# Performance work log

Hardware: AMD Instinct MI355X
Metric: run time of the kernel (lower is better)

Reference implementation:

```python
import jax, jax.numpy as jnp
import numpy as np

PRED_LEN = 256
K = 32
LOW_FREQ = 1


def setup_inputs() -> dict:
    key = jax.random.key(0)
    x = jax.random.normal(key, (8, 1024, 512), dtype=jnp.float32)
    return {"x": x}


def _fourier_layer(x):
    b, t, d = x.shape
    # per-channel standardization over time (torch .std is unbiased -> ddof=1)
    x_mean = jnp.mean(x, axis=1, keepdims=True)                      # (b,1,d)
    x_std = jnp.std(x, axis=1, keepdims=True, ddof=1) + 1e-8         # (b,1,d)
    xs = jnp.clip((x - x_mean) / x_std, -2.0, 2.0) + 1e-9

    # rfft over time; t is even and LOW_FREQ < t//2 -> drop DC..low_freq-1 and Nyquist
    x_freq = jnp.fft.rfft(xs, axis=1)[:, LOW_FREQ:-1]                # (b,N,d) complex64
    n_freq = x_freq.shape[1]
    f = jnp.fft.rfftfreq(t).astype(jnp.float32)[LOW_FREQ:n_freq + LOW_FREQ]  # (N,)

    # top-k frequencies by amplitude, independently per (batch, channel)
    amp_all = jnp.abs(x_freq).astype(jnp.float32)                    # (b,N,d)
    _, idx = jax.lax.top_k(jnp.transpose(amp_all, (0, 2, 1)), K)     # (b,d,k)
    idx = jnp.transpose(idx, (0, 2, 1))                              # (b,k,d)
    xf = jnp.take_along_axis(x_freq, idx, axis=1)                    # (b,k,d)
    f_sel = f[idx]                                                   # (b,k,d)

    # extrapolate: conjugate pair -> real signal, sum of k cosines
    xf2 = jnp.concatenate([xf, jnp.conj(xf)], axis=1)                # (b,2k,d)
    f2 = jnp.concatenate([f_sel, -f_sel], axis=1)[:, :, None, :]     # (b,2k,1,d)
    T = t + PRED_LEN
    t_val = jnp.arange(T, dtype=jnp.float32)[None, None, :, None]    # (1,1,T,1)
    amp = (jnp.abs(xf2) / (t + 1e-8))[:, :, None, :]                 # (b,2k,1,d)
    phase = jnp.clip(jnp.angle(xf2), -np.pi, np.pi)[:, :, None, :]   # (b,2k,1,d)
    angle = 2.0 * np.pi * f2 * t_val + phase                         # (b,2k,T,d)
    angle = angle - 2.0 * np.pi * jnp.floor(angle / (2.0 * np.pi))
    x_time = jnp.sum(amp * jnp.cos(angle), axis=1)                   # (b,T,d)

    return x_time * x_std + x_mean


def reference(x):
    return _fourier_layer(x)
```

## Files before the change

kernel.cpp:

```cpp
#include <hip/hip_runtime.h>

#define T_IN 1024
#define D_DIM 512
#define T_OUT 1280
#define NPAIR 4096

__global__ __launch_bounds__(256) void transpose_kernel(const float* __restrict__ x,
                                                        float* __restrict__ xt,
                                                        double2* __restrict__ tw) {
    __shared__ float tile[64][65];
    const int b  = blockIdx.z;
    const int t0 = blockIdx.y * 64;
    const int d0 = blockIdx.x * 64;
    const int dl = threadIdx.x & 63;
    const int r0 = threadIdx.x >> 6;

    if (blockIdx.x < 4 && blockIdx.y == 0 && blockIdx.z == 0) {
        int m = blockIdx.x * 256 + threadIdx.x;
        double th = (6.283185307179586476925286766559 / 1024.0) * (double)m;
        tw[m] = make_double2(cos(th), -sin(th));
    }

#pragma unroll
    for (int i = 0; i < 16; ++i) {
        int tl = r0 * 16 + i;
        tile[tl][dl] = x[((size_t)b * T_IN + (t0 + tl)) * D_DIM + d0 + dl];
    }
    __syncthreads();
#pragma unroll
    for (int i = 0; i < 16; ++i) {
        int dl2 = r0 * 16 + i;
        xt[((size_t)b * D_DIM + (d0 + dl2)) * T_IN + t0 + dl] = tile[dl][dl2];
    }
}

__device__ __forceinline__ double2 TW16(const double2* __restrict__ E, int m) {
    const double RS2 = 0.70710678118654752440084436210485;
    int r = m & 255;
    int q = (m >> 8) & 3;
    int r2 = (r <= 128) ? r : 256 - r;
    double cc, ss;
    if (r2 <= 64) {
        double2 t = E[r2];
        cc = t.x; ss = t.y;
    } else {
        double2 t = E[128 - r2];
        cc = (t.x + t.y) * RS2;
        ss = (t.x - t.y) * RS2;
    }
    double c, s;
    if (r > 128) { c = ss; s = cc; } else { c = cc; s = ss; }
    double C, S;
    switch (q) {
        case 0:  C = c;  S = s;  break;
        case 1:  C = -s; S = c;  break;
        case 2:  C = -c; S = -s; break;
        default: C = s;  S = -c; break;
    }
    return make_double2(C, -S);
}

__global__ __launch_bounds__(256) void dft_kernel(const float* __restrict__ xt,
                                                  const double2* __restrict__ twg,
                                                  float2* __restrict__ stats,
                                                  float4* __restrict__ sel) {
    __shared__ double2 uni[1024];
    __shared__ double2 tw_s[65];
    __shared__ double2 w32_s[32];
    __shared__ double  red_s[16];
    double* xs_s = (double*)uni;

    const int tid  = threadIdx.x;
    const int pair = blockIdx.x;

    const float4 v = reinterpret_cast<const float4*>(xt + (size_t)pair * T_IN)[tid];

    if (tid < 65) {
        double2 t = twg[tid];
        tw_s[tid] = make_double2(t.x, -t.y);
    }
    if (tid >= 128 && tid < 160) {
        w32_s[tid - 128] = twg[(tid - 128) * 32];
    }

    double sum = (double)v.x + (double)v.y + (double)v.z + (double)v.w;
    double sq  = (double)v.x * v.x + (double)v.y * v.y +
                 (double)v.z * v.z + (double)v.w * v.w;
#pragma unroll
    for (int off = 32; off; off >>= 1) {
        sum += __shfl_down(sum, off);
        sq  += __shfl_down(sq, off);
    }
    const int wv   = tid >> 6;
    const int lane = tid & 63;
    if (lane == 0) { red_s[wv] = sum; red_s[8 + wv] = sq; }
    __syncthreads();
    double mean, stdp;
    {
        double s = red_s[0] + red_s[1] + red_s[2] + red_s[3];
        double q = red_s[8] + red_s[9] + red_s[10] + red_s[11];
        mean = s * (1.0 / 1024.0);
        double var = (q - 1024.0 * mean * mean) * (1.0 / 1023.0);
        var = var > 0.0 ? var : 0.0;
        stdp = sqrt(var) + 1e-8;
        if (tid == 0) stats[pair] = make_float2((float)mean, (float)stdp);
    }
    const double inv = 1.0 / stdp;
    {
        double z0 = ((double)v.x - mean) * inv;
        double z1 = ((double)v.y - mean) * inv;
        double z2 = ((double)v.z - mean) * inv;
        double z3 = ((double)v.w - mean) * inv;
        z0 = fmin(2.0, fmax(-2.0, z0)) + 1e-9;
        z1 = fmin(2.0, fmax(-2.0, z1)) + 1e-9;
        z2 = fmin(2.0, fmax(-2.0, z2)) + 1e-9;
        z3 = fmin(2.0, fmax(-2.0, z3)) + 1e-9;
        xs_s[tid * 4 + 0] = z0;
        xs_s[tid * 4 + 1] = z1;
        xs_s[tid * 4 + 2] = z2;
        xs_s[tid * 4 + 3] = z3;
    }
    __syncthreads();

    {
        int idx = tid;
#pragma unroll
        for (int rr = 0; rr < 2; ++rr) {
            if (idx < 480) {
                int t1p = 1 + (idx >> 5);
                int t2c = idx & 31;
                int ia = t1p * 32 + t2c;
                int ib = (32 - t1p) * 32 + t2c;
                double a = xs_s[ia], b = xs_s[ib];
                xs_s[ia] = a + b;
                xs_s[ib] = a - b;
            }
            idx += 256;
        }
    }
    __syncthreads();

    const int k1 = tid & 31;
    const int g  = tid >> 5;

    double2 R0, R1, R2, R3;
    {
        const double sgn16 = (k1 & 1) ? -1.0 : 1.0;

        double ar0 = xs_s[g]      + sgn16 * xs_s[512 + g];
        double ar1 = xs_s[g + 8]  + sgn16 * xs_s[512 + g + 8];
        double ar2 = xs_s[g + 16] + sgn16 * xs_s[512 + g + 16];
        double ar3 = xs_s[g + 24] + sgn16 * xs_s[512 + g + 24];
        double ai0 = 0, ai1 = 0, ai2 = 0, ai3 = 0;

        int jw = 0;
#pragma unroll 5
        for (int t1 = 1; t1 <= 15; ++t1) {
            jw = (jw + k1) & 31;
            double2 w = w32_s[jw];
            const double* eb = &xs_s[t1 * 32];
            const double* ob = &xs_s[(32 - t1) * 32];
            ar0 = fma(eb[g], w.x, ar0);      ai0 = fma(ob[g], w.y, ai0);
            ar1 = fma(eb[g + 8], w.x, ar1);  ai1 = fma(ob[g + 8], w.y, ai1);
            ar2 = fma(eb[g + 16], w.x, ar2); ai2 = fma(ob[g + 16], w.y, ai2);
            ar3 = fma(eb[g + 24], w.x, ar3); ai3 = fma(ob[g + 24], w.y, ai3);
        }
        {
            double2 tm = TW16(tw_s, g * k1);
            R0 = make_double2(ar0 * tm.x - ai0 * tm.y, ar0 * tm.y + ai0 * tm.x);
        }
        {
            double2 tm = TW16(tw_s, (g + 8) * k1);
            R1 = make_double2(ar1 * tm.x - ai1 * tm.y, ar1 * tm.y + ai1 * tm.x);
        }
        {
            double2 tm = TW16(tw_s, (g + 16) * k1);
            R2 = make_double2(ar2 * tm.x - ai2 * tm.y, ar2 * tm.y + ai2 * tm.x);
        }
        {
            double2 tm = TW16(tw_s, (g + 24) * k1);
            R3 = make_double2(ar3 * tm.x - ai3 * tm.y, ar3 * tm.y + ai3 * tm.x);
        }
    }
    __syncthreads();

    uni[g * 32 + k1]        = make_double2(R0.x + R2.x, R0.y + R2.y);
    uni[(g + 16) * 32 + k1] = make_double2(R0.x - R2.x, R0.y - R2.y);
    uni[(g + 8) * 32 + k1]  = make_double2(R1.x + R3.x, R1.y + R3.y);
    uni[(g + 24) * 32 + k1] = make_double2(R1.x - R3.x, R1.y - R3.y);
    __syncthreads();

    double Ar = 0, Ai = 0, Br = 0, Bi = 0;
    {
        const int ebase = (g & 1) ? 16 * 32 : 0;
        int ja = 0;
#pragma unroll
        for (int u = 0; u < 4; ++u) {
            {
                double2 w = w32_s[ja]; ja = (ja + g) & 31;
                double2 E = uni[ebase + (4 * u + 0) * 32 + k1];
                double P = fma(E.x, w.x, -(E.y * w.y));
                double Q = fma(E.x, w.y,  (E.y * w.x));
                Ar += P; Ai += Q; Br += P; Bi += Q;
            }
            {
                double2 w = w32_s[ja]; ja = (ja + g) & 31;
                double2 E = uni[ebase + (4 * u + 1) * 32 + k1];
                double P = fma(E.x, w.x, -(E.y * w.y));
                double Q = fma(E.x, w.y,  (E.y * w.x));
                Ar += P; Ai += Q; Br += Q; Bi -= P;
            }
            {
                double2 w = w32_s[ja]; ja = (ja + g) & 31;
                double2 E = uni[ebase + (4 * u + 2) * 32 + k1];
                double P = fma(E.x, w.x, -(E.y * w.y));
                double Q = fma(E.x, w.y,  (E.y * w.x));
                Ar += P; Ai += Q; Br -= P; Bi -= Q;
            }
            {
                double2 w = w32_s[ja]; ja = (ja + g) & 31;
                double2 E = uni[ebase + (4 * u + 3) * 32 + k1];
                double P = fma(E.x, w.x, -(E.y * w.y));
                double Q = fma(E.x, w.y,  (E.y * w.x));
                Ar += P; Ai += Q; Br -= Q; Bi += P;
            }
        }
    }
    const int ka = k1 + 32 * g;
    const int kb = ka + 256;

    unsigned long long uA, uB;
    {
        double a2a = Ar * Ar + Ai * Ai;
        double a2b = Br * Br + Bi * Bi;
        unsigned long long bba = __double_as_longlong(a2a);
        unsigned long long bbb = __double_as_longlong(a2b);
        double keya = __longlong_as_double((bba & ~1023ULL) |
                                           (unsigned long long)(1023 - ka));
        double keyb = __longlong_as_double((bbb & ~1023ULL) |
                                           (unsigned long long)(1023 - kb));
        if (ka == 0) keya = -1.0;
        unsigned long long a = (unsigned long long)__double_as_longlong(keya);
        unsigned long long b = (unsigned long long)__double_as_longlong(keyb);
        uA = a ^ ((a >> 63) ? 0xFFFFFFFFFFFFFFFFULL : 0x8000000000000000ULL);
        uB = b ^ ((b >> 63) ? 0xFFFFFFFFFFFFFFFFULL : 0x8000000000000000ULL);
    }

    __syncthreads();
    float2* spec_f = (float2*)uni;
    double* cand   = (double*)(uni + 512);
    spec_f[ka] = make_float2((float)Ar, (float)Ai);
    spec_f[kb] = make_float2((float)Br, (float)Bi);

    const unsigned long long lt = lane ? (0xFFFFFFFFFFFFFFFFULL >> (64 - lane))
                                       : 0ULL;

    {
        const unsigned int aHi = (unsigned int)(uA >> 32);
        const unsigned int bHi = (unsigned int)(uB >> 32);
        unsigned int pref = 0x80000000u;
#pragma unroll
        for (int bit = 30; bit >= 0; --bit) {
            unsigned int trial = pref | (1u << bit);
            int cnt = __popcll(__ballot(aHi >= trial)) +
                      __popcll(__ballot(bHi >= trial));
            if (cnt >= 32) pref = trial;
        }
        unsigned long long gA = __ballot(aHi > pref);
        unsigned long long gB = __ballot(bHi > pref);
        unsigned long long eA = __ballot(aHi == pref);
        unsigned long long eB = __ballot(bHi == pref);
        int nH = __popcll(gA) + __popcll(gB);
        int nE = __popcll(eA) + __popcll(eB);
        bool winA, winB;
        if (nH + nE == 32) {
            winA = (aHi >= pref);
            winB = (bHi >= pref);
        } else {
            const unsigned int aLo = (unsigned int)uA;
            const unsigned int bLo = (unsigned int)uB;
            int need = 32 - nH;
            unsigned int lp = 0;
            for (int bit = 31; bit >= 0; --bit) {
                unsigned int t = lp | (1u << bit);
                int c = __popcll(__ballot((aHi == pref) && (aLo >= t))) +
                        __popcll(__ballot((bHi == pref) && (bLo >= t)));
                if (c >= need) lp = t;
            }
            winA = (aHi > pref) || ((aHi == pref) && (aLo >= lp));
            winB = (bHi > pref) || ((bHi == pref) && (bLo >= lp));
        }
        unsigned long long mA = __ballot(winA);
        unsigned long long mB = __ballot(winB);
        const int bs = wv * 32;
        if (winA)
            cand[bs + __popcll(mA & lt)] = __longlong_as_double((long long)uA);
        if (winB)
            cand[bs + __popcll(mA) + __popcll(mB & lt)] =
                __longlong_as_double((long long)uB);
    }
    __syncthreads();

    if (tid < 64) {
        unsigned long long c0 =
            (unsigned long long)__double_as_longlong(cand[tid]);
        unsigned long long c1 =
            (unsigned long long)__double_as_longlong(cand[tid + 64]);
        const unsigned int h0 = (unsigned int)(c0 >> 32);
        const unsigned int h1 = (unsigned int)(c1 >> 32);
        unsigned int pref = 0x80000000u;
#pragma unroll
        for (int bit = 30; bit >= 0; --bit) {
            unsigned int trial = pref | (1u << bit);
            int cnt = __popcll(__ballot(h0 >= trial)) +
                      __popcll(__ballot(h1 >= trial));
            if (cnt >= 32) pref = trial;
        }
        unsigned long long g0 = __ballot(h0 > pref);
        unsigned long long g1 = __ballot(h1 > pref);
        unsigned long long e0 = __ballot(h0 == pref);
        unsigned long long e1 = __ballot(h1 == pref);
        int nH = __popcll(g0) + __popcll(g1);
        int nE = __popcll(e0) + __popcll(e1);
        bool win0, win1;
        if (nH + nE == 32) {
            win0 = (h0 >= pref);
            win1 = (h1 >= pref);
        } else {
            const unsigned int l0 = (unsigned int)c0;
            const unsigned int l1 = (unsigned int)c1;
            int need = 32 - nH;
            unsigned int lp = 0;
            for (int bit = 31; bit >= 0; --bit) {
                unsigned int t = lp | (1u << bit);
                int c = __popcll(__ballot((h0 == pref) && (l0 >= t))) +
                        __popcll(__ballot((h1 == pref) && (l1 >= t)));
                if (c >= need) lp = t;
            }
            win0 = (h0 > pref) || ((h0 == pref) && (l0 >= lp));
            win1 = (h1 > pref) || ((h1 == pref) && (l1 >= lp));
        }
        unsigned long long m0 = __ballot(win0);
        unsigned long long m1 = __ballot(win1);
        const float C = 6.28318530717958647692f / 1024.0f;
        const size_t sb = (size_t)pair * 32;
        if (win0) {
            int slot = __popcll(m0 & lt);
            int k = 1023 - (int)(c0 & 1023ULL);
            float2 sp = spec_f[k];
            float ph = atan2f(sp.y, sp.x);
            double key = __longlong_as_double(
                (long long)(c0 ^ 0x8000000000000000ULL));
            double amp = sqrt(key);
            float aout = (float)(2.0 * amp / (1024.0 + 1e-8));
            float tkc = __cosf((float)k * C);
            sel[sb + slot] = make_float4(aout, ph, (float)k, tkc);
        }
        if (win1) {
            int slot = __popcll(m0) + __popcll(m1 & lt);
            int k = 1023 - (int)(c1 & 1023ULL);
            float2 sp = spec_f[k];
            float ph = atan2f(sp.y, sp.x);
            double key = __longlong_as_double(
                (long long)(c1 ^ 0x8000000000000000ULL));
            double amp = sqrt(key);
            float aout = (float)(2.0 * amp / (1024.0 + 1e-8));
            float tkc = __cosf((float)k * C);
            sel[sb + slot] = make_float4(aout, ph, (float)k, tkc);
        }
    }
}

__global__ __launch_bounds__(256) void recon_kernel(const float4* __restrict__ sel,
                                                    const float2* __restrict__ stats,
                                                    float* __restrict__ out) {
    __shared__ float4 sel_s[32][65];
    __shared__ float2 st_s[64];
    const int bid   = blockIdx.x;
    const int chunk = bid & 15;
    const int dt    = (bid >> 4) & 7;
    const int b     = bid >> 7;
    const int d0    = dt * 64;
    const int tid   = threadIdx.x;
#pragma unroll
    for (int it = 0; it < 8; ++it) {
        int i   = tid + it * 256;
        int j   = i & 31;
        int dls = i >> 5;
        sel_s[j][dls] = sel[((size_t)(b * D_DIM + d0 + dls)) * 32 + j];
    }
    if (tid < 64) st_s[tid] = stats[b * D_DIM + d0 + tid];
    __syncthreads();

    const int dl    = tid & 63;
    const int wvv   = tid >> 6;
    const int tbase = chunk * 64 + wvv * 16;

    float acc[16];
#pragma unroll
    for (int j = 0; j < 16; ++j) acc[j] = 0.0f;

    const float C = 6.28318530717958647692f / 1024.0f;
#pragma unroll 2
    for (int js = 0; js < 32; ++js) {
        float4 tr = sel_s[js][dl];
        const float a = tr.x;
        int k = (int)tr.z;
        float ck = tr.w;
        float sk = sqrtf(fmaxf(1.0f - ck * ck, 0.0f));
        int mm0 = (k * tbase) & 1023;
        float ang0 = fmaf((float)mm0, C, tr.y);
        float s0, c0;
        __sincosf(ang0, &s0, &c0);
        float c1 = c0 * ck - s0 * sk;
        float K2 = ck + ck;
        acc[0] = fmaf(a, c0, acc[0]);
        acc[1] = fmaf(a, c1, acc[1]);
#pragma unroll
        for (int j = 2; j < 16; ++j) {
            float c2 = fmaf(K2, c1, -c0);
            acc[j] = fmaf(a, c2, acc[j]);
            c0 = c1; c1 = c2;
        }
    }
    const float2 st = st_s[dl];
#pragma unroll
    for (int j = 0; j < 16; ++j) {
        float o = fmaf(acc[j], st.y, st.x);
        int t = tbase + j;
        out[((size_t)b * T_OUT + t) * D_DIM + d0 + dl] = o;
        if (t < 256)
            out[((size_t)b * T_OUT + t + 1024) * D_DIM + d0 + dl] = o;
    }
}

extern "C" void kernel_launch(void* const* d_in, const int* in_sizes, int n_in,
                              void* d_out, int out_size, void* d_ws, size_t ws_size,
                              hipStream_t stream) {
    const float* x = (const float*)d_in[0];
    float* out = (float*)d_out;
    char* ws = (char*)d_ws;
    const size_t MB = 1024 * 1024;

    float*   xt    = (float*)ws;
    double2* tw    = (double2*)(ws + 16 * MB);
    float2*  stats = (float2*)(ws + 16 * MB + 65536);
    float4*  sel   = (float4*)(ws + 16 * MB + 131072);

    transpose_kernel<<<dim3(8, 16, 8), 256, 0, stream>>>(x, xt, tw);
    dft_kernel<<<NPAIR, 256, 0, stream>>>(xt, tw, stats, sel);
    recon_kernel<<<1024, 256, 0, stream>>>(sel, stats, out);
}
```

Before: 68.02 us.

## Run DFT and top-k in fp32 with fp64 fallback for ambiguous selections

Adds a float32 version of the per-channel DFT and top-k selection kernel, which writes results and a per-pair flag. The flag is set when the gap between the smallest selected and the largest rejected amplitude is too small to trust. The original double-precision kernel then runs only for flagged pairs and returns early for the rest. The aim is to cut expensive fp64 arithmetic on MI355X, at the cost of an extra kernel launch and a precision-dependent fallback path.

```diff
diff --git a/kernel.cpp b/kernel.cpp
--- a/kernel.cpp
+++ b/kernel.cpp
@@ -7,7 +7,9 @@
 
 __global__ __launch_bounds__(256) void transpose_kernel(const float* __restrict__ x,
                                                         float* __restrict__ xt,
-                                                        double2* __restrict__ tw) {
+                                                        double2* __restrict__ tw,
+                                                        float2* __restrict__ tw16f,
+                                                        float2* __restrict__ w32f) {
     __shared__ float tile[64][65];
     const int b  = blockIdx.z;
     const int t0 = blockIdx.y * 64;
@@ -18,7 +20,10 @@
     if (blockIdx.x < 4 && blockIdx.y == 0 && blockIdx.z == 0) {
         int m = blockIdx.x * 256 + threadIdx.x;
         double th = (6.283185307179586476925286766559 / 1024.0) * (double)m;
-        tw[m] = make_double2(cos(th), -sin(th));
+        double c = cos(th), s = sin(th);
+        tw[m] = make_double2(c, -s);
+        if (m <= 64)       tw16f[m]      = make_float2((float)c, (float)s);
+        if ((m & 31) == 0) w32f[m >> 5]  = make_float2((float)c, (float)(-s));
     }
 
 #pragma unroll
@@ -60,10 +65,371 @@
     return make_double2(C, -S);
 }
 
-__global__ __launch_bounds__(256) void dft_kernel(const float* __restrict__ xt,
-                                                  const double2* __restrict__ twg,
-                                                  float2* __restrict__ stats,
-                                                  float4* __restrict__ sel) {
+__device__ __forceinline__ float2 TW16F(const float2* __restrict__ E, int m) {
+    const float RS2 = 0.70710678118654752440f;
+    int r = m & 255;
+    int q = (m >> 8) & 3;
+    int r2 = (r <= 128) ? r : 256 - r;
+    float cc, ss;
+    if (r2 <= 64) {
+        float2 t = E[r2];
+        cc = t.x; ss = t.y;
+    } else {
+        float2 t = E[128 - r2];
+        cc = (t.x + t.y) * RS2;
+        ss = (t.x - t.y) * RS2;
+    }
+    float c, s;
+    if (r > 128) { c = ss; s = cc; } else { c = cc; s = ss; }
+    float C, S;
+    switch (q) {
+        case 0:  C = c;  S = s;  break;
+        case 1:  C = -s; S = c;  break;
+        case 2:  C = -c; S = -s; break;
+        default: C = s;  S = -c; break;
+    }
+    return make_float2(C, -S);
+}
+
+__global__ __launch_bounds__(256) void dft32_kernel(const float* __restrict__ xt,
+                                                    const float2* __restrict__ tw16fg,
+                                                    const float2* __restrict__ w32fg,
+                                                    float2* __restrict__ stats,
+                                                    float4* __restrict__ sel,
+                                                    int* __restrict__ flag) {
+    __shared__ float2 uni[1024];
+    __shared__ float2 tw_s[65];
+    __shared__ float2 w32_s[32];
+    __shared__ double red_s[16];
+    float* xs_f = (float*)uni;
+
+    const int tid  = threadIdx.x;
+    const int pair = blockIdx.x;
+
+    const float4 v = reinterpret_cast<const float4*>(xt + (size_t)pair * T_IN)[tid];
+
+    if (tid < 65) tw_s[tid] = tw16fg[tid];
+    if (tid >= 128 && tid < 160) w32_s[tid - 128] = w32fg[tid - 128];
+
+    double sum = (double)v.x + (double)v.y + (double)v.z + (double)v.w;
+    double sq  = (double)v.x * v.x + (double)v.y * v.y +
+                 (double)v.z * v.z + (double)v.w * v.w;
+#pragma unroll
+    for (int off = 32; off; off >>= 1) {
+        sum += __shfl_down(sum, off);
+        sq  += __shfl_down(sq, off);
+    }
+    const int wv   = tid >> 6;
+    const int lane = tid & 63;
+    if (lane == 0) { red_s[wv] = sum; red_s[8 + wv] = sq; }
+    __syncthreads();
+    double mean, stdp;
+    {
+        double s = red_s[0] + red_s[1] + red_s[2] + red_s[3];
+        double q = red_s[8] + red_s[9] + red_s[10] + red_s[11];
+        mean = s * (1.0 / 1024.0);
+        double var = (q - 1024.0 * mean * mean) * (1.0 / 1023.0);
+        var = var > 0.0 ? var : 0.0;
+        stdp = sqrt(var) + 1e-8;
+        if (tid == 0) stats[pair] = make_float2((float)mean, (float)stdp);
+    }
+    const double inv = 1.0 / stdp;
+    {
+        double z0 = ((double)v.x - mean) * inv;
+        double z1 = ((double)v.y - mean) * inv;
+        double z2 = ((double)v.z - mean) * inv;
+        double z3 = ((double)v.w - mean) * inv;
+        z0 = fmin(2.0, fmax(-2.0, z0)) + 1e-9;
+        z1 = fmin(2.0, fmax(-2.0, z1)) + 1e-9;
+        z2 = fmin(2.0, fmax(-2.0, z2)) + 1e-9;
+        z3 = fmin(2.0, fmax(-2.0, z3)) + 1e-9;
+        xs_f[tid * 4 + 0] = (float)z0;
+        xs_f[tid * 4 + 1] = (float)z1;
+        xs_f[tid * 4 + 2] = (float)z2;
+        xs_f[tid * 4 + 3] = (float)z3;
+    }
+    __syncthreads();
+
+    {
+        int idx = tid;
+#pragma unroll
+        for (int rr = 0; rr < 2; ++rr) {
+            if (idx < 480) {
+                int t1p = 1 + (idx >> 5);
+                int t2c = idx & 31;
+                int ia = t1p * 32 + t2c;
+                int ib = (32 - t1p) * 32 + t2c;
+                float a = xs_f[ia], b = xs_f[ib];
+                xs_f[ia] = a + b;
+                xs_f[ib] = a - b;
+            }
+            idx += 256;
+        }
+    }
+    __syncthreads();
+
+    const int k1 = tid & 31;
+    const int g  = tid >> 5;
+
+    float2 R0, R1, R2, R3;
+    {
+        const float sgn16 = (k1 & 1) ? -1.0f : 1.0f;
+
+        float ar0 = xs_f[g]      + sgn16 * xs_f[512 + g];
+        float ar1 = xs_f[g + 8]  + sgn16 * xs_f[512 + g + 8];
+        float ar2 = xs_f[g + 16] + sgn16 * xs_f[512 + g + 16];
+        float ar3 = xs_f[g + 24] + sgn16 * xs_f[512 + g + 24];
+        float ai0 = 0, ai1 = 0, ai2 = 0, ai3 = 0;
+
+        int jw = 0;
+#pragma unroll 5
+        for (int t1 = 1; t1 <= 15; ++t1) {
+            jw = (jw + k1) & 31;
+            float2 w = w32_s[jw];
+            const float* eb = &xs_f[t1 * 32];
+            const float* ob = &xs_f[(32 - t1) * 32];
+            ar0 = fmaf(eb[g], w.x, ar0);      ai0 = fmaf(ob[g], w.y, ai0);
+            ar1 = fmaf(eb[g + 8], w.x, ar1);  ai1 = fmaf(ob[g + 8], w.y, ai1);
+            ar2 = fmaf(eb[g + 16], w.x, ar2); ai2 = fmaf(ob[g + 16], w.y, ai2);
+            ar3 = fmaf(eb[g + 24], w.x, ar3); ai3 = fmaf(ob[g + 24], w.y, ai3);
+        }
+        {
+            float2 tm = TW16F(tw_s, g * k1);
+            R0 = make_float2(ar0 * tm.x - ai0 * tm.y, ar0 * tm.y + ai0 * tm.x);
+        }
+        {
+            float2 tm = TW16F(tw_s, (g + 8) * k1);
+            R1 = make_float2(ar1 * tm.x - ai1 * tm.y, ar1 * tm.y + ai1 * tm.x);
+        }
+        {
+            float2 tm = TW16F(tw_s, (g + 16) * k1);
+            R2 = make_float2(ar2 * tm.x - ai2 * tm.y, ar2 * tm.y + ai2 * tm.x);
+        }
+        {
+            float2 tm = TW16F(tw_s, (g + 24) * k1);
+            R3 = make_float2(ar3 * tm.x - ai3 * tm.y, ar3 * tm.y + ai3 * tm.x);
+        }
+    }
+    __syncthreads();
+
+    uni[g * 32 + k1]        = make_float2(R0.x + R2.x, R0.y + R2.y);
+    uni[(g + 16) * 32 + k1] = make_float2(R0.x - R2.x, R0.y - R2.y);
+    uni[(g + 8) * 32 + k1]  = make_float2(R1.x + R3.x, R1.y + R3.y);
+    uni[(g + 24) * 32 + k1] = make_float2(R1.x - R3.x, R1.y - R3.y);
+    __syncthreads();
+
+    float Ar = 0, Ai = 0, Br = 0, Bi = 0;
+    {
+        const int ebase = (g & 1) ? 16 * 32 : 0;
+        int ja = 0;
+#pragma unroll
+        for (int u = 0; u < 4; ++u) {
+            {
+                float2 w = w32_s[ja]; ja = (ja + g) & 31;
+                float2 E = uni[ebase + (4 * u + 0) * 32 + k1];
+                float P = fmaf(E.x, w.x, -(E.y * w.y));
+                float Q = fmaf(E.x, w.y,  (E.y * w.x));
+                Ar += P; Ai += Q; Br += P; Bi += Q;
+            }
+            {
+                float2 w = w32_s[ja]; ja = (ja + g) & 31;
+                float2 E = uni[ebase + (4 * u + 1) * 32 + k1];
+                float P = fmaf(E.x, w.x, -(E.y * w.y));
+                float Q = fmaf(E.x, w.y,  (E.y * w.x));
+                Ar += P; Ai += Q; Br += Q; Bi -= P;
+            }
+            {
+                float2 w = w32_s[ja]; ja = (ja + g) & 31;
+                float2 E = uni[ebase + (4 * u + 2) * 32 + k1];
+                float P = fmaf(E.x, w.x, -(E.y * w.y));
+                float Q = fmaf(E.x, w.y,  (E.y * w.x));
+                Ar += P; Ai += Q; Br -= P; Bi -= Q;
+            }
+            {
+                float2 w = w32_s[ja]; ja = (ja + g) & 31;
+                float2 E = uni[ebase + (4 * u + 3) * 32 + k1];
+                float P = fmaf(E.x, w.x, -(E.y * w.y));
+                float Q = fmaf(E.x, w.y,  (E.y * w.x));
+                Ar += P; Ai += Q; Br -= Q; Bi += P;
+            }
+        }
+    }
+    const int ka = k1 + 32 * g;
+    const int kb = ka + 256;
+
+    unsigned long long uA, uB;
+    {
+        float a2a = Ar * Ar + Ai * Ai;
+        float a2b = Br * Br + Bi * Bi;
+        uA = ((unsigned long long)__float_as_uint(a2a) << 32) |
+             (unsigned int)(1023 - ka);
+        uB = ((unsigned long long)__float_as_uint(a2b) << 32) |
+             (unsigned int)(1023 - kb);
+        if (ka == 0) uA = 0;
+    }
+
+    __syncthreads();
+    float2* spec_f = (float2*)uni;
+    unsigned long long* cand = (unsigned long long*)(uni + 512);
+    spec_f[ka] = make_float2(Ar, Ai);
+    spec_f[kb] = make_float2(Br, Bi);
+
+    const unsigned long long lt = lane ? (0xFFFFFFFFFFFFFFFFULL >> (64 - lane))
+                                       : 0ULL;
+
+    {
+        const unsigned int aHi = (unsigned int)(uA >> 32);
+        const unsigned int bHi = (unsigned int)(uB >> 32);
+        unsigned int pref = 0;
+#pragma unroll
+        for (int bit = 31; bit >= 0; --bit) {
+            unsigned int trial = pref | (1u << bit);
+            int cnt = __popcll(__ballot(aHi >= trial)) +
+                      __popcll(__ballot(bHi >= trial));
+            if (cnt >= 33) pref = trial;
+        }
+        unsigned long long gA = __ballot(aHi > pref);
+        unsigned long long gB = __ballot(bHi > pref);
+        unsigned long long eA = __ballot(aHi == pref);
+        unsigned long long eB = __ballot(bHi == pref);
+        int nH = __popcll(gA) + __popcll(gB);
+        int nE = __popcll(eA) + __popcll(eB);
+        bool winA, winB;
+        if (nH + nE == 33) {
+            winA = (aHi >= pref);
+            winB = (bHi >= pref);
+        } else {
+            const unsigned int aLo = (unsigned int)uA;
+            const unsigned int bLo = (unsigned int)uB;
+            int need = 33 - nH;
+            unsigned int lp = 0;
+            for (int bit = 31; bit >= 0; --bit) {
+                unsigned int t = lp | (1u << bit);
+                int c = __popcll(__ballot((aHi == pref) && (aLo >= t))) +
+                        __popcll(__ballot((bHi == pref) && (bLo >= t)));
+                if (c >= need) lp = t;
+            }
+            winA = (aHi > pref) || ((aHi == pref) && (aLo >= lp));
+            winB = (bHi > pref) || ((bHi == pref) && (bLo >= lp));
+        }
+        unsigned long long mA = __ballot(winA);
+        unsigned long long mB = __ballot(winB);
+        const int bs = wv * 33;
+        if (winA) cand[bs + __popcll(mA & lt)] = uA;
+        if (winB) cand[bs + __popcll(mA) + __popcll(mB & lt)] = uB;
+    }
+    __syncthreads();
+
+    if (tid < 64) {
+        unsigned long long c0 = cand[tid];
+        unsigned long long c1 = cand[tid + 64];
+        unsigned long long c2 = (tid < 4) ? cand[128 + tid] : 0ULL;
+        const unsigned int h0 = (unsigned int)(c0 >> 32);
+        const unsigned int h1 = (unsigned int)(c1 >> 32);
+        const unsigned int h2 = (unsigned int)(c2 >> 32);
+        unsigned int pref = 0;
+#pragma unroll
+        for (int bit = 31; bit >= 0; --bit) {
+            unsigned int trial = pref | (1u << bit);
+            int cnt = __popcll(__ballot(h0 >= trial)) +
+                      __popcll(__ballot(h1 >= trial)) +
+                      __popcll(__ballot(h2 >= trial));
+            if (cnt >= 32) pref = trial;
+        }
+        unsigned long long g0 = __ballot(h0 > pref);
+        unsigned long long g1 = __ballot(h1 > pref);
+        unsigned long long g2 = __ballot(h2 > pref);
+        unsigned long long e0 = __ballot(h0 == pref);
+        unsigned long long e1 = __ballot(h1 == pref);
+        unsigned long long e2 = __ballot(h2 == pref);
+        int nH = __popcll(g0) + __popcll(g1) + __popcll(g2);
+        int nE = __popcll(e0) + __popcll(e1) + __popcll(e2);
+        bool win0, win1, win2;
+        if (nH + nE == 32) {
+            win0 = (h0 >= pref);
+            win1 = (h1 >= pref);
+            win2 = (h2 >= pref);
+        } else {
+            const unsigned int l0 = (unsigned int)c0;
+            const unsigned int l1 = (unsigned int)c1;
+            const unsigned int l2 = (unsigned int)c2;
+            int need = 32 - nH;
+            unsigned int lp = 0;
+            for (int bit = 31; bit >= 0; --bit) {
+                unsigned int t = lp | (1u << bit);
+                int c = __popcll(__ballot((h0 == pref) && (l0 >= t))) +
+                        __popcll(__ballot((h1 == pref) && (l1 >= t))) +
+                        __popcll(__ballot((h2 == pref) && (l2 >= t)));
+                if (c >= need) lp = t;
+            }
+            win0 = (h0 > pref) || ((h0 == pref) && (l0 >= lp));
+            win1 = (h1 > pref) || ((h1 == pref) && (l1 >= lp));
+            win2 = (h2 > pref) || ((h2 == pref) && (l2 >= lp));
+        }
+        float minW = 3.4e38f, maxL = 0.0f;
+        {
+            float a2 = __uint_as_float(h0);
+            if (win0) minW = fminf(minW, a2); else maxL = fmaxf(maxL, a2);
+        }
+        {
+            float a2 = __uint_as_float(h1);
+            if (win1) minW = fminf(minW, a2); else maxL = fmaxf(maxL, a2);
+        }
+        {
+            float a2 = __uint_as_float(h2);
+            if (win2) minW = fminf(minW, a2); else maxL = fmaxf(maxL, a2);
+        }
+#pragma unroll
+        for (int off = 1; off < 64; off <<= 1) {
+            minW = fminf(minW, __shfl_xor(minW, off));
+            maxL = fmaxf(maxL, __shfl_xor(maxL, off));
+        }
+        if (tid == 0)
+            flag[pair] = ((minW - maxL) < 1e-3f * minW) ? 1 : 0;
+
+        unsigned long long m0 = __ballot(win0);
+        unsigned long long m1 = __ballot(win1);
+        unsigned long long m2 = __ballot(win2);
+        const float C = 6.28318530717958647692f / 1024.0f;
+        const size_t sb = (size_t)pair * 32;
+        if (win0) {
+            int slot = __popcll(m0 & lt);
+            int k = 1023 - (int)(c0 & 0xFFFFFFFFULL);
+            float2 sp = spec_f[k];
+            float ph = atan2f(sp.y, sp.x);
+            float aout = 2.0f * sqrtf(__uint_as_float(h0)) * (1.0f / 1024.0f);
+            float tkc = __cosf((float)k * C);
+            sel[sb + slot] = make_float4(aout, ph, (float)k, tkc);
+        }
+        if (win1) {
+            int slot = __popcll(m0) + __popcll(m1 & lt);
+            int k = 1023 - (int)(c1 & 0xFFFFFFFFULL);
+            float2 sp = spec_f[k];
+            float ph = atan2f(sp.y, sp.x);
+            float aout = 2.0f * sqrtf(__uint_as_float(h1)) * (1.0f / 1024.0f);
+            float tkc = __cosf((float)k * C);
+            sel[sb + slot] = make_float4(aout, ph, (float)k, tkc);
+        }
+        if (win2) {
+            int slot = __popcll(m0) + __popcll(m1) + __popcll(m2 & lt);
+            int k = 1023 - (int)(c2 & 0xFFFFFFFFULL);
+            float2 sp = spec_f[k];
+            float ph = atan2f(sp.y, sp.x);
+            float aout = 2.0f * sqrtf(__uint_as_float(h2)) * (1.0f / 1024.0f);
+            float tkc = __cosf((float)k * C);
+            sel[sb + slot] = make_float4(aout, ph, (float)k, tkc);
+        }
+    }
+}
+
+__global__ __launch_bounds__(256) void dft64_kernel(const float* __restrict__ xt,
+                                                    const double2* __restrict__ twg,
+                                                    float2* __restrict__ stats,
+                                                    float4* __restrict__ sel,
+                                                    const int* __restrict__ flag) {
+    const int pair = blockIdx.x;
+    if (flag[pair] == 0) return;
+
     __shared__ double2 uni[1024];
     __shared__ double2 tw_s[65];
     __shared__ double2 w32_s[32];
@@ -71,7 +437,6 @@
     double* xs_s = (double*)uni;
 
     const int tid  = threadIdx.x;
-    const int pair = blockIdx.x;
 
     const float4 v = reinterpret_cast<const float4*>(xt + (size_t)pair * T_IN)[tid];
 
@@ -444,10 +809,14 @@
 
     float*   xt    = (float*)ws;
     double2* tw    = (double2*)(ws + 16 * MB);
-    float2*  stats = (float2*)(ws + 16 * MB + 65536);
+    float2*  tw16f = (float2*)(ws + 16 * MB + 65536);
+    float2*  w32f  = (float2*)(ws + 16 * MB + 69632);
+    float2*  stats = (float2*)(ws + 16 * MB + 73728);
+    int*     flag  = (int*)(ws + 16 * MB + 106496);
     float4*  sel   = (float4*)(ws + 16 * MB + 131072);
 
-    transpose_kernel<<<dim3(8, 16, 8), 256, 0, stream>>>(x, xt, tw);
-    dft_kernel<<<NPAIR, 256, 0, stream>>>(xt, tw, stats, sel);
+    transpose_kernel<<<dim3(8, 16, 8), 256, 0, stream>>>(x, xt, tw, tw16f, w32f);
+    dft32_kernel<<<NPAIR, 256, 0, stream>>>(xt, tw16f, w32f, stats, sel, flag);
+    dft64_kernel<<<NPAIR, 256, 0, stream>>>(xt, tw, stats, sel, flag);
     recon_kernel<<<1024, 256, 0, stream>>>(sel, stats, out);
 }
```

Result: slower. 75.26 us (+10.6%).
